# Performance work log

Measured on AMD Instinct MI355X. Metric: run time of the kernel, lower is better.

## Reference

```python
import jax, jax.numpy as jnp
import numpy as np

HIDDEN = 64
IN_SIZE = 2048 + 512  # sum(obs_shape) + sum(action_shape)


def setup_inputs() -> dict:
    key = jax.random.key(0)
    ks = jax.random.split(key, 10)
    B = 32768
    s_in = 1.0 / np.sqrt(IN_SIZE)
    s_h = 1.0 / np.sqrt(HIDDEN)
    return {
        "state": jax.random.normal(ks[0], (B, 2048), dtype=jnp.float32),
        "action": jax.random.normal(ks[1], (B, 512), dtype=jnp.float32),
        "hidden_state": jax.random.normal(ks[2], (B, HIDDEN), dtype=jnp.float32),
        "cell_state": jax.random.normal(ks[3], (B, HIDDEN), dtype=jnp.float32),
        # fused gate weights, gate order: [i, f, g, o]
        "Wi": jax.random.uniform(ks[4], (IN_SIZE, 4 * HIDDEN), jnp.float32, -s_in, s_in),
        "bi": jax.random.uniform(ks[5], (4 * HIDDEN,), jnp.float32, -s_in, s_in),
        "Wh": jax.random.uniform(ks[6], (HIDDEN, 4 * HIDDEN), jnp.float32, -s_h, s_h),
        "bh": jax.random.uniform(ks[7], (4 * HIDDEN,), jnp.float32, -s_h, s_h),
        "Wo": jax.random.uniform(ks[8], (HIDDEN, 1), jnp.float32, -s_h, s_h),
        "bo": jax.random.uniform(ks[9], (1,), jnp.float32, -s_h, s_h),
    }


def reference(state, action, hidden_state, cell_state, Wi, bi, Wh, bh, Wo, bo):
    x = jnp.concatenate([state, action], axis=1)  # [B, IN_SIZE]
    # two fused GEMMs covering all 8 Linear layers (gate order i,f,g,o)
    gates = x @ Wi + bi + hidden_state @ Wh + bh  # [B, 4*HIDDEN]
    i_t, f_t, g_t, o_t = jnp.split(gates, 4, axis=1)
    i_t = jax.nn.sigmoid(i_t)
    f_t = jax.nn.sigmoid(f_t)
    g_t = jnp.tanh(g_t)
    o_t = jax.nn.sigmoid(o_t)
    c_t = f_t * cell_state + i_t * g_t
    h_t = o_t * jnp.tanh(c_t)
    out = jnp.tanh(h_t @ Wo + bo)  # [B, 1]
    return (out, h_t, c_t)
```

## Files before the change

kernel.cpp:

```cpp
#include <hip/hip_runtime.h>
#include <hip/hip_bf16.h>

#define K_IN 2624
#define NGATE 256
#define LDS_A_STRIDE 72
#define SMEM_BYTES 41984

typedef __attribute__((ext_vector_type(8))) short short8;
typedef __attribute__((ext_vector_type(4))) short short4_t;
typedef __attribute__((ext_vector_type(4))) float float4_t;

__device__ __forceinline__ short f2bf(float f) {
    union { __hip_bfloat16 b; short s; } u;
    u.b = __float2bfloat16(f);
    return u.s;
}

__device__ __forceinline__ float sigmoid_fast(float x) {
    return 1.f / (1.f + __expf(-x));
}

__device__ __forceinline__ float tanh_fast(float x) {
    float e = __expf(-2.f * fabsf(x));
    float t = (1.f - e) / (1.f + e);
    return copysignf(t, x);
}

__global__ void prep_kernel(const float* __restrict__ Wi, const float* __restrict__ bi,
                            const float* __restrict__ Wh, const float* __restrict__ bh,
                            short* __restrict__ Wt, float* __restrict__ bsum) {
    __shared__ short tile[64][256];
    const int t = threadIdx.x;
    const int kb = blockIdx.x;
    const int k0 = kb * 64;

    for (int j = 0; j < 64; ++j) {
        int k = k0 + j;
        float v = (k < 2560) ? Wi[(size_t)k * 256 + t] : Wh[(size_t)(k - 2560) * 256 + t];
        tile[j][t] = f2bf(v);
    }
    if (kb == 0) bsum[t] = bi[t] + bh[t];
    __syncthreads();

    const int j0 = (t >> 6) * 16;
    for (int q = 0; q < 4; ++q) {
        int n = (t & 63) + 64 * q;
        short8 v0, v1;
#pragma unroll
        for (int jj = 0; jj < 8; ++jj) v0[jj] = tile[j0 + jj][n];
#pragma unroll
        for (int jj = 0; jj < 8; ++jj) v1[jj] = tile[j0 + 8 + jj][n];
        short* dst = Wt + (size_t)n * K_IN + k0 + j0;
        *reinterpret_cast<short8*>(dst) = v0;
        *reinterpret_cast<short8*>(dst + 8) = v1;
    }
}

__global__ __launch_bounds__(256, 3)
void lstm_kernel(const float* __restrict__ state, const float* __restrict__ action,
                 const float* __restrict__ hidden, const float* __restrict__ cell,
                 const short* __restrict__ Wt, const float* __restrict__ bsum,
                 const float* __restrict__ Wo, const float* __restrict__ bo,
                 float* __restrict__ out, int Brows) {
    __shared__ __align__(16) char smem[SMEM_BYTES];
    short* sA = (short*)smem;
    short* sB = (short*)(smem + 9216);
    float* sG = (float*)smem;

    const int t = threadIdx.x;
    const int w = t >> 6;
    const int l = t & 63;
    const int bm = blockIdx.x;

    const int ar = t >> 4;
    const int ac = (t & 15) * 4;

    int boff[8];
#pragma unroll
    for (int p = 0; p < 8; ++p) {
        int n = (p * 4 + w) * 8 + (l >> 3);
        int jg = (l & 7) ^ (n & 7);
        boff[p] = n * K_IN + jg * 8;
    }

    float4_t acc[4][4];
#pragma unroll
    for (int i = 0; i < 4; ++i)
#pragma unroll
        for (int j = 0; j < 4; ++j) acc[i][j] = (float4_t)(0.f);

    float4_t areg[4];
#pragma unroll
    for (int p = 0; p < 4; ++p) {
        size_t row = (size_t)bm * 64 + ar + p * 16;
        areg[p] = *reinterpret_cast<const float4_t*>(state + (row << 11) + ac);
    }

    for (int it = 0; it < 41; ++it) {
        const int k0 = it * 64;

#pragma unroll
        for (int p = 0; p < 8; ++p) {
            __builtin_amdgcn_global_load_lds(
                (const __attribute__((address_space(1))) void*)(Wt + boff[p] + k0),
                (__attribute__((address_space(3))) void*)(sB + (p * 4 + w) * 512),
                16, 0, 0);
        }

#pragma unroll
        for (int p = 0; p < 4; ++p) {
            short4_t s4;
            s4[0] = f2bf(areg[p][0]); s4[1] = f2bf(areg[p][1]);
            s4[2] = f2bf(areg[p][2]); s4[3] = f2bf(areg[p][3]);
            *reinterpret_cast<short4_t*>(sA + (ar + p * 16) * LDS_A_STRIDE + ac) = s4;
        }

        if (it + 1 < 41) {
            int k1 = k0 + 64;
            const float* src; int shift; int c0;
            if (k1 < 2048)      { src = state;  shift = 11; c0 = k1; }
            else if (k1 < 2560) { src = action; shift = 9;  c0 = k1 - 2048; }
            else                { src = hidden; shift = 6;  c0 = k1 - 2560; }
#pragma unroll
            for (int p = 0; p < 4; ++p) {
                size_t row = (size_t)bm * 64 + ar + p * 16;
                areg[p] = *reinterpret_cast<const float4_t*>(src + (row << shift) + c0 + ac);
            }
        }

        __syncthreads();

#pragma unroll
        for (int ks = 0; ks < 2; ++ks) {
            short8 afrag[4], bfrag[4];
#pragma unroll
            for (int mt = 0; mt < 4; ++mt) {
                int m = mt * 16 + (l & 15);
                afrag[mt] = *reinterpret_cast<short8*>(sA + m * LDS_A_STRIDE + ks * 32 + (l >> 4) * 8);
            }
#pragma unroll
            for (int nt = 0; nt < 4; ++nt) {
                int n = w * 64 + nt * 16 + (l & 15);
                int chunk = (ks * 4 + (l >> 4)) ^ (l & 7);
                bfrag[nt] = *reinterpret_cast<short8*>(sB + n * 64 + chunk * 8);
            }
#pragma unroll
            for (int mt = 0; mt < 4; ++mt)
#pragma unroll
                for (int nt = 0; nt < 4; ++nt)
                    acc[mt][nt] = __builtin_amdgcn_mfma_f32_16x16x32_bf16(
                        afrag[mt], bfrag[nt], acc[mt][nt], 0, 0, 0);
        }

        __syncthreads();
    }

    float* outH = out + Brows;
    float* outC = out + Brows + (size_t)Brows * 64;
    const float wo = Wo[l];
    const float bov = bo[0];
    const float b0 = bsum[l];
    const float b1 = bsum[64 + l];
    const float b2 = bsum[128 + l];
    const float b3 = bsum[192 + l];

#pragma unroll
    for (int ph = 0; ph < 2; ++ph) {
#pragma unroll
        for (int mh = 0; mh < 2; ++mh) {
            int mt = ph * 2 + mh;
#pragma unroll
            for (int nt = 0; nt < 4; ++nt) {
#pragma unroll
                for (int r = 0; r < 4; ++r) {
                    int row = mh * 16 + (l >> 4) * 4 + r;
                    int col = w * 64 + nt * 16 + (l & 15);
                    sG[row * 260 + col] = acc[mt][nt][r];
                }
            }
        }
        __syncthreads();

#pragma unroll
        for (int q = 0; q < 8; ++q) {
            int rr = w * 8 + q;
            size_t gr = (size_t)bm * 64 + ph * 32 + rr;
            float gi = sG[rr * 260 + l]       + b0;
            float gf = sG[rr * 260 + 64 + l]  + b1;
            float gg = sG[rr * 260 + 128 + l] + b2;
            float go = sG[rr * 260 + 192 + l] + b3;
            float i_t = sigmoid_fast(gi);
            float f_t = sigmoid_fast(gf);
            float g_t = tanh_fast(gg);
            float o_t = sigmoid_fast(go);
            float c_old = cell[gr * 64 + l];
            float c_t = f_t * c_old + i_t * g_t;
            float h_t = o_t * tanh_fast(c_t);
            outC[gr * 64 + l] = c_t;
            outH[gr * 64 + l] = h_t;
            float v = h_t * wo;
#pragma unroll
            for (int off = 32; off > 0; off >>= 1) v += __shfl_down(v, off);
            if (l == 0) out[gr] = tanh_fast(v + bov);
        }
        __syncthreads();
    }
}

extern "C" void kernel_launch(void* const* d_in, const int* in_sizes, int n_in,
                              void* d_out, int out_size, void* d_ws, size_t ws_size,
                              hipStream_t stream) {
    const float* state  = (const float*)d_in[0];
    const float* action = (const float*)d_in[1];
    const float* hidden = (const float*)d_in[2];
    const float* cell   = (const float*)d_in[3];
    const float* Wi     = (const float*)d_in[4];
    const float* bi     = (const float*)d_in[5];
    const float* Wh     = (const float*)d_in[6];
    const float* bh     = (const float*)d_in[7];
    const float* Wo     = (const float*)d_in[8];
    const float* bo     = (const float*)d_in[9];

    const int Brows = in_sizes[0] / 2048;

    short* Wt   = (short*)d_ws;
    float* bsum = (float*)((char*)d_ws + (size_t)NGATE * K_IN * sizeof(short));

    prep_kernel<<<K_IN / 64, 256, 0, stream>>>(Wi, bi, Wh, bh, Wt, bsum);
    lstm_kernel<<<Brows / 64, 256, 0, stream>>>(state, action, hidden, cell,
                                                Wt, bsum, Wo, bo, (float*)d_out, Brows);
}
```

Baseline: 467.3 us.

## Rewrite LSTM GEMM as single-wave blocks with register-resident pre-swizzled weights

Reorganizes the weight prep to emit B in MFMA fragment order per 32-wide K step, so each lane loads its fragments straight from global memory into registers without LDS staging. The main kernel now uses one 64-thread wave per 16-row tile, streams A directly from global memory with nontemporal loads, and software-pipelines one step ahead in registers. The aim is to remove the LDS round-trips and block-wide barriers. In exchange, each wave re-reads the full weight matrix (relying on L2), issues many more blocks, and carries high register pressure from 16 prefetched B fragments.

```diff
diff --git a/kernel.cpp b/kernel.cpp
--- a/kernel.cpp
+++ b/kernel.cpp
@@ -2,12 +2,9 @@
 #include <hip/hip_bf16.h>
 
 #define K_IN 2624
-#define NGATE 256
-#define LDS_A_STRIDE 72
-#define SMEM_BYTES 41984
+#define NSTEP 82
 
 typedef __attribute__((ext_vector_type(8))) short short8;
-typedef __attribute__((ext_vector_type(4))) short short4_t;
 typedef __attribute__((ext_vector_type(4))) float float4_t;
 
 __device__ __forceinline__ short f2bf(float f) {
@@ -28,182 +25,141 @@
 
 __global__ void prep_kernel(const float* __restrict__ Wi, const float* __restrict__ bi,
                             const float* __restrict__ Wh, const float* __restrict__ bh,
-                            short* __restrict__ Wt, float* __restrict__ bsum) {
-    __shared__ short tile[64][256];
+                            short* __restrict__ Wt2, float* __restrict__ bsum) {
+    __shared__ short tile[32][264];
     const int t = threadIdx.x;
     const int kb = blockIdx.x;
-    const int k0 = kb * 64;
+    const int k0 = kb * 32;
 
-    for (int j = 0; j < 64; ++j) {
+#pragma unroll 8
+    for (int j = 0; j < 32; ++j) {
         int k = k0 + j;
-        float v = (k < 2560) ? Wi[(size_t)k * 256 + t] : Wh[(size_t)(k - 2560) * 256 + t];
+        float v = (k < 2560) ? Wi[(size_t)k * 256 + t]
+                             : Wh[(size_t)(k - 2560) * 256 + t];
         tile[j][t] = f2bf(v);
     }
     if (kb == 0) bsum[t] = bi[t] + bh[t];
     __syncthreads();
 
-    const int j0 = (t >> 6) * 16;
-    for (int q = 0; q < 4; ++q) {
-        int n = (t & 63) + 64 * q;
-        short8 v0, v1;
 #pragma unroll
-        for (int jj = 0; jj < 8; ++jj) v0[jj] = tile[j0 + jj][n];
+    for (int c = 0; c < 4; ++c) {
+        int idx = c * 256 + t;
+        int lane = idx & 63;
+        int nb = idx >> 6;
+        int n = nb * 16 + (lane & 15);
+        int j0 = (lane >> 4) * 8;
+        short8 v;
 #pragma unroll
-        for (int jj = 0; jj < 8; ++jj) v1[jj] = tile[j0 + 8 + jj][n];
-        short* dst = Wt + (size_t)n * K_IN + k0 + j0;
-        *reinterpret_cast<short8*>(dst) = v0;
-        *reinterpret_cast<short8*>(dst + 8) = v1;
+        for (int j = 0; j < 8; ++j) v[j] = tile[j0 + j][n];
+        *reinterpret_cast<short8*>(Wt2 + (size_t)kb * 8192 + (size_t)idx * 8) = v;
     }
 }
 
-__global__ __launch_bounds__(256, 3)
+__global__ __launch_bounds__(64, 2)
 void lstm_kernel(const float* __restrict__ state, const float* __restrict__ action,
                  const float* __restrict__ hidden, const float* __restrict__ cell,
-                 const short* __restrict__ Wt, const float* __restrict__ bsum,
+                 const short* __restrict__ Wt2, const float* __restrict__ bsum,
                  const float* __restrict__ Wo, const float* __restrict__ bo,
                  float* __restrict__ out, int Brows) {
-    __shared__ __align__(16) char smem[SMEM_BYTES];
-    short* sA = (short*)smem;
-    short* sB = (short*)(smem + 9216);
-    float* sG = (float*)smem;
+    __shared__ float sG[16 * 260];
 
-    const int t = threadIdx.x;
-    const int w = t >> 6;
-    const int l = t & 63;
+    const int l = threadIdx.x;
     const int bm = blockIdx.x;
+    const int lr = l & 15;
+    const int q = l >> 4;
 
-    const int ar = t >> 4;
-    const int ac = (t & 15) * 4;
+    const size_t mrow = (size_t)bm * 16 + lr;
+    const float* aS = state  + mrow * 2048 + q * 8;
+    const float* aA = action + mrow * 512  + q * 8;
+    const float* aH = hidden + mrow * 64   + q * 8;
+    const short* bP = Wt2 + (size_t)l * 8;
 
-    int boff[8];
+    float4_t acc[16];
 #pragma unroll
-    for (int p = 0; p < 8; ++p) {
-        int n = (p * 4 + w) * 8 + (l >> 3);
-        int jg = (l & 7) ^ (n & 7);
-        boff[p] = n * K_IN + jg * 8;
+    for (int nb = 0; nb < 16; ++nb) acc[nb] = (float4_t)(0.f);
+
+    short8 Bc[16];
+    float4_t Ac0, Ac1;
+#pragma unroll
+    for (int nb = 0; nb < 16; ++nb)
+        Bc[nb] = *reinterpret_cast<const short8*>(bP + nb * 512);
+    Ac0 = __builtin_nontemporal_load(reinterpret_cast<const float4_t*>(aS));
+    Ac1 = __builtin_nontemporal_load(reinterpret_cast<const float4_t*>(aS + 4));
+
+#pragma unroll 2
+    for (int s = 0; s < 81; ++s) {
+        short8 Bn[16];
+        float4_t An0, An1;
+        const short* bp1 = bP + (size_t)(s + 1) * 8192;
+#pragma unroll
+        for (int nb = 0; nb < 16; ++nb)
+            Bn[nb] = *reinterpret_cast<const short8*>(bp1 + nb * 512);
+        {
+            int sn = s + 1;
+            const float* p;
+            int col;
+            if (sn < 64)      { p = aS; col = sn * 32; }
+            else if (sn < 80) { p = aA; col = (sn - 64) * 32; }
+            else              { p = aH; col = (sn - 80) * 32; }
+            An0 = __builtin_nontemporal_load(reinterpret_cast<const float4_t*>(p + col));
+            An1 = __builtin_nontemporal_load(reinterpret_cast<const float4_t*>(p + col + 4));
+        }
+
+        short8 a;
+        a[0] = f2bf(Ac0[0]); a[1] = f2bf(Ac0[1]); a[2] = f2bf(Ac0[2]); a[3] = f2bf(Ac0[3]);
+        a[4] = f2bf(Ac1[0]); a[5] = f2bf(Ac1[1]); a[6] = f2bf(Ac1[2]); a[7] = f2bf(Ac1[3]);
+#pragma unroll
+        for (int nb = 0; nb < 16; ++nb)
+            acc[nb] = __builtin_amdgcn_mfma_f32_16x16x32_bf16(a, Bc[nb], acc[nb], 0, 0, 0);
+
+#pragma unroll
+        for (int nb = 0; nb < 16; ++nb) Bc[nb] = Bn[nb];
+        Ac0 = An0; Ac1 = An1;
+    }
+    {
+        short8 a;
+        a[0] = f2bf(Ac0[0]); a[1] = f2bf(Ac0[1]); a[2] = f2bf(Ac0[2]); a[3] = f2bf(Ac0[3]);
+        a[4] = f2bf(Ac1[0]); a[5] = f2bf(Ac1[1]); a[6] = f2bf(Ac1[2]); a[7] = f2bf(Ac1[3]);
+#pragma unroll
+        for (int nb = 0; nb < 16; ++nb)
+            acc[nb] = __builtin_amdgcn_mfma_f32_16x16x32_bf16(a, Bc[nb], acc[nb], 0, 0, 0);
     }
 
-    float4_t acc[4][4];
 #pragma unroll
-    for (int i = 0; i < 4; ++i)
+    for (int nb = 0; nb < 16; ++nb)
 #pragma unroll
-        for (int j = 0; j < 4; ++j) acc[i][j] = (float4_t)(0.f);
+        for (int r = 0; r < 4; ++r)
+            sG[(q * 4 + r) * 260 + nb * 16 + lr] = acc[nb][r];
+    __syncthreads();
 
-    float4_t areg[4];
-#pragma unroll
-    for (int p = 0; p < 4; ++p) {
-        size_t row = (size_t)bm * 64 + ar + p * 16;
-        areg[p] = *reinterpret_cast<const float4_t*>(state + (row << 11) + ac);
-    }
-
-    for (int it = 0; it < 41; ++it) {
-        const int k0 = it * 64;
-
-#pragma unroll
-        for (int p = 0; p < 8; ++p) {
-            __builtin_amdgcn_global_load_lds(
-                (const __attribute__((address_space(1))) void*)(Wt + boff[p] + k0),
-                (__attribute__((address_space(3))) void*)(sB + (p * 4 + w) * 512),
-                16, 0, 0);
-        }
-
-#pragma unroll
-        for (int p = 0; p < 4; ++p) {
-            short4_t s4;
-            s4[0] = f2bf(areg[p][0]); s4[1] = f2bf(areg[p][1]);
-            s4[2] = f2bf(areg[p][2]); s4[3] = f2bf(areg[p][3]);
-            *reinterpret_cast<short4_t*>(sA + (ar + p * 16) * LDS_A_STRIDE + ac) = s4;
-        }
-
-        if (it + 1 < 41) {
-            int k1 = k0 + 64;
-            const float* src; int shift; int c0;
-            if (k1 < 2048)      { src = state;  shift = 11; c0 = k1; }
-            else if (k1 < 2560) { src = action; shift = 9;  c0 = k1 - 2048; }
-            else                { src = hidden; shift = 6;  c0 = k1 - 2560; }
-#pragma unroll
-            for (int p = 0; p < 4; ++p) {
-                size_t row = (size_t)bm * 64 + ar + p * 16;
-                areg[p] = *reinterpret_cast<const float4_t*>(src + (row << shift) + c0 + ac);
-            }
-        }
-
-        __syncthreads();
-
-#pragma unroll
-        for (int ks = 0; ks < 2; ++ks) {
-            short8 afrag[4], bfrag[4];
-#pragma unroll
-            for (int mt = 0; mt < 4; ++mt) {
-                int m = mt * 16 + (l & 15);
-                afrag[mt] = *reinterpret_cast<short8*>(sA + m * LDS_A_STRIDE + ks * 32 + (l >> 4) * 8);
-            }
-#pragma unroll
-            for (int nt = 0; nt < 4; ++nt) {
-                int n = w * 64 + nt * 16 + (l & 15);
-                int chunk = (ks * 4 + (l >> 4)) ^ (l & 7);
-                bfrag[nt] = *reinterpret_cast<short8*>(sB + n * 64 + chunk * 8);
-            }
-#pragma unroll
-            for (int mt = 0; mt < 4; ++mt)
-#pragma unroll
-                for (int nt = 0; nt < 4; ++nt)
-                    acc[mt][nt] = __builtin_amdgcn_mfma_f32_16x16x32_bf16(
-                        afrag[mt], bfrag[nt], acc[mt][nt], 0, 0, 0);
-        }
-
-        __syncthreads();
-    }
-
-    float* outH = out + Brows;
-    float* outC = out + Brows + (size_t)Brows * 64;
     const float wo = Wo[l];
     const float bov = bo[0];
     const float b0 = bsum[l];
     const float b1 = bsum[64 + l];
     const float b2 = bsum[128 + l];
     const float b3 = bsum[192 + l];
+    float* outH = out + Brows;
+    float* outC = outH + (size_t)Brows * 64;
 
 #pragma unroll
-    for (int ph = 0; ph < 2; ++ph) {
+    for (int r = 0; r < 16; ++r) {
+        size_t grow = (size_t)bm * 16 + r;
+        float gi = sG[r * 260 + l]       + b0;
+        float gf = sG[r * 260 + 64 + l]  + b1;
+        float gg = sG[r * 260 + 128 + l] + b2;
+        float go = sG[r * 260 + 192 + l] + b3;
+        float i_t = sigmoid_fast(gi);
+        float f_t = sigmoid_fast(gf);
+        float g_t = tanh_fast(gg);
+        float o_t = sigmoid_fast(go);
+        float c_t = f_t * cell[grow * 64 + l] + i_t * g_t;
+        float h_t = o_t * tanh_fast(c_t);
+        outC[grow * 64 + l] = c_t;
+        outH[grow * 64 + l] = h_t;
+        float v = h_t * wo;
 #pragma unroll
-        for (int mh = 0; mh < 2; ++mh) {
-            int mt = ph * 2 + mh;
-#pragma unroll
-            for (int nt = 0; nt < 4; ++nt) {
-#pragma unroll
-                for (int r = 0; r < 4; ++r) {
-                    int row = mh * 16 + (l >> 4) * 4 + r;
-                    int col = w * 64 + nt * 16 + (l & 15);
-                    sG[row * 260 + col] = acc[mt][nt][r];
-                }
-            }
-        }
-        __syncthreads();
-
-#pragma unroll
-        for (int q = 0; q < 8; ++q) {
-            int rr = w * 8 + q;
-            size_t gr = (size_t)bm * 64 + ph * 32 + rr;
-            float gi = sG[rr * 260 + l]       + b0;
-            float gf = sG[rr * 260 + 64 + l]  + b1;
-            float gg = sG[rr * 260 + 128 + l] + b2;
-            float go = sG[rr * 260 + 192 + l] + b3;
-            float i_t = sigmoid_fast(gi);
-            float f_t = sigmoid_fast(gf);
-            float g_t = tanh_fast(gg);
-            float o_t = sigmoid_fast(go);
-            float c_old = cell[gr * 64 + l];
-            float c_t = f_t * c_old + i_t * g_t;
-            float h_t = o_t * tanh_fast(c_t);
-            outC[gr * 64 + l] = c_t;
-            outH[gr * 64 + l] = h_t;
-            float v = h_t * wo;
-#pragma unroll
-            for (int off = 32; off > 0; off >>= 1) v += __shfl_down(v, off);
-            if (l == 0) out[gr] = tanh_fast(v + bov);
-        }
-        __syncthreads();
+        for (int off = 32; off > 0; off >>= 1) v += __shfl_down(v, off);
+        if (l == 0) out[grow] = tanh_fast(v + bov);
     }
 }
 
@@ -223,10 +179,10 @@
 
     const int Brows = in_sizes[0] / 2048;
 
-    short* Wt   = (short*)d_ws;
-    float* bsum = (float*)((char*)d_ws + (size_t)NGATE * K_IN * sizeof(short));
+    short* Wt2  = (short*)d_ws;
+    float* bsum = (float*)((char*)d_ws + (size_t)NSTEP * 8192 * sizeof(short));
 
-    prep_kernel<<<K_IN / 64, 256, 0, stream>>>(Wi, bi, Wh, bh, Wt, bsum);
-    lstm_kernel<<<Brows / 64, 256, 0, stream>>>(state, action, hidden, cell,
-                                                Wt, bsum, Wo, bo, (float*)d_out, Brows);
+    prep_kernel<<<NSTEP, 256, 0, stream>>>(Wi, bi, Wh, bh, Wt2, bsum);
+    lstm_kernel<<<Brows / 16, 64, 0, stream>>>(state, action, hidden, cell,
+                                               Wt2, bsum, Wo, bo, (float*)d_out, Brows);
 }
```

Measured after the change: 542.8 us. 1.16x slower.
